# Optimization experiments

Hardware: AMD Instinct MI355X
Metric: run time of the kernel (lower is better)

The kernel has to match this reference:

```python
import jax, jax.numpy as jnp
import numpy as np

N_NODES = 100000
N_EDGES = 1200000
FEAT = 64
AVG_D_LOG = float(np.log(13.0))  # log(avg_degree + 1), avg_degree = 12
EPS_STD = 1e-5   # PNA std epsilon
EPS_BN = 1e-5    # torch BatchNorm1d default eps


def setup_inputs() -> dict:
    key = jax.random.key(0)
    k_h, k_norm, k_src, k_dst = jax.random.split(key, 4)
    h = jax.random.normal(k_h, (N_NODES, FEAT), dtype=jnp.float32)
    norm = jax.random.uniform(k_norm, (N_NODES, 1), dtype=jnp.float32)
    e = jnp.zeros((N_EDGES, 1), dtype=jnp.float32)  # unused by the layer
    src = jax.random.randint(k_src, (N_EDGES,), 0, N_NODES, dtype=jnp.int32)
    dst = jnp.sort(jax.random.randint(k_dst, (N_EDGES,), 0, N_NODES, dtype=jnp.int32))
    bn_weight = jnp.ones((FEAT,), dtype=jnp.float32)
    bn_bias = jnp.zeros((FEAT,), dtype=jnp.float32)
    return {"h": h, "norm": norm, "e": e, "bn_weight": bn_weight,
            "bn_bias": bn_bias, "src": src, "dst": dst}


def reference(h, norm, e, bn_weight, bn_bias, src, dst):
    N, F = h.shape
    hn = h * norm                           # [N, F] pre-scaled node features
    m = hn[src]                             # [E, F] gathered messages (copy_u)

    ones = jnp.ones_like(dst, dtype=hn.dtype)
    deg = jax.ops.segment_sum(ones, dst, num_segments=N, indices_are_sorted=True)  # [N]
    deg_safe = jnp.maximum(deg, 1.0)
    has_nb = (deg > 0)[:, None]             # zero in-degree nodes get zeros (DGL)

    s1 = jax.ops.segment_sum(m, dst, num_segments=N, indices_are_sorted=True)
    s2 = jax.ops.segment_sum(m * m, dst, num_segments=N, indices_are_sorted=True)
    mean = s1 / deg_safe[:, None]
    var = jax.nn.relu(s2 / deg_safe[:, None] - mean * mean)
    std = jnp.sqrt(var + EPS_STD)
    mx = jnp.where(has_nb, jax.ops.segment_max(m, dst, num_segments=N, indices_are_sorted=True), 0.0)
    mn = jnp.where(has_nb, jax.ops.segment_min(m, dst, num_segments=N, indices_are_sorted=True), 0.0)

    agg = jnp.concatenate([mean, mx, mn, std], axis=1)          # [N, 4F]

    logD = jnp.log(deg + 1.0)[:, None]                           # [N, 1]
    amp = agg * (logD / AVG_D_LOG)                               # amplification scaler
    att = agg * (AVG_D_LOG / jnp.where(logD > 0, logD, 1.0))     # attenuation scaler
    scaled = jnp.concatenate([agg, amp, att], axis=1)            # [N, 12F]
    scaled = jnp.where(has_nb, scaled, 0.0)

    out = jnp.concatenate([hn, scaled * norm], axis=1)           # [N, 13F]
    out = out.reshape(N, 13, F).mean(axis=1)                     # [N, F]
    out = jax.nn.relu(out)                                       # activation (dropout p=0)

    # BatchNorm1d, training mode (biased batch variance), affine
    mu = out.mean(axis=0)
    v = out.var(axis=0)
    out = (out - mu) / jnp.sqrt(v + EPS_BN) * bn_weight + bn_bias
    return out
```

## Files before the change

### kernel.cpp

```cpp
#include <hip/hip_runtime.h>
#include <hip/hip_fp16.h>
#include <math.h>
#include <float.h>

#define N_NODES 100000
#define N_EDGES 1200000
#define FEAT 64
#define AVG_D_LOG 2.5649493574615367f
#define EPS_STD 1e-5f
#define EPS_BN 1e-5
#define AGG_BLOCKS 12500
#define HN_BLOCKS 6250
#define RP_BLOCKS 391
#define OLD_RED_BLOCKS 512

#if __has_builtin(__builtin_fmaxf16)
#define H16MAX(a,b) __builtin_fmaxf16((a),(b))
#define H16MIN(a,b) __builtin_fminf16((a),(b))
#else
#define H16MAX(a,b) ((a) > (b) ? (a) : (b))
#define H16MIN(a,b) ((a) < (b) ? (a) : (b))
#endif

__global__ void __launch_bounds__(256) hn_rowptr(
    const float* __restrict__ h, const float* __restrict__ norm,
    const int* __restrict__ dst,
    __half* __restrict__ hn_h, int* __restrict__ rowptr)
{
    const int b = blockIdx.x;
    if (b < HN_BLOCKS) {
        const size_t i4 = ((size_t)b * 256 + threadIdx.x) * 4;
        const int node = (int)(i4 >> 6);
        const float nr = norm[node];
        float4 v = *reinterpret_cast<const float4*>(h + i4);
        __half2 p0 = __floats2half2_rn(v.x * nr, v.y * nr);
        __half2 p1 = __floats2half2_rn(v.z * nr, v.w * nr);
        __half2* o = reinterpret_cast<__half2*>(hn_h + i4);
        o[0] = p0; o[1] = p1;
    } else {
        const int n = (b - HN_BLOCKS) * 256 + threadIdx.x;
        if (n > N_NODES) return;
        int lo = 0, hi = N_EDGES;
        while (lo < hi) {
            int mid = (lo + hi) >> 1;
            if (dst[mid] < n) lo = mid + 1; else hi = mid;
        }
        rowptr[n] = lo;
    }
}

template <bool WRITE_PSTAT>
__global__ void __launch_bounds__(256) pna_agg6(
    const __half* __restrict__ hn, const float* __restrict__ norm,
    const int* __restrict__ src, const int* __restrict__ rowptr,
    float* __restrict__ out, float2* __restrict__ pstat)
{
    const int tid  = threadIdx.x;
    const int wid  = tid >> 6;
    const int lane = tid & 63;
    const int n0   = (blockIdx.x * 4 + wid) * 2;

    const int s0 = __builtin_amdgcn_readfirstlane(rowptr[n0]);
    const int e0 = __builtin_amdgcn_readfirstlane(rowptr[n0 + 1]);
    const int e1 = __builtin_amdgcn_readfirstlane(rowptr[n0 + 2]);
    const int degA = e0 - s0;
    const int degB = e1 - e0;

    const _Float16* __restrict__ hnf = (const _Float16*)hn;
    const float ownA = (float)hnf[(size_t)n0 * FEAT + lane];
    const float ownB = (float)hnf[(size_t)(n0 + 1) * FEAT + lane];

    float s1A = 0.f, s2A = 0.f, s1B = 0.f, s2B = 0.f;
    _Float16 mxA = (_Float16)(-65504.f), mnA = (_Float16)(65504.f);
    _Float16 mxB = (_Float16)(-65504.f), mnB = (_Float16)(65504.f);

#define LOADW(J)  (hnf[(size_t)(J) * FEAT + lane])
#define ACCA(W) do { _Float16 w_ = (W); float f_ = (float)w_;                 \
                     s1A = __builtin_fmaf(f_, 1.0f, s1A);                     \
                     s2A = __builtin_fmaf(f_, f_, s2A);                       \
                     mxA = H16MAX(mxA, w_); mnA = H16MIN(mnA, w_); } while (0)
#define ACCB(W) do { _Float16 w_ = (W); float f_ = (float)w_;                 \
                     s1B = __builtin_fmaf(f_, 1.0f, s1B);                     \
                     s2B = __builtin_fmaf(f_, f_, s2B);                       \
                     mxB = H16MAX(mxB, w_); mnB = H16MIN(mnB, w_); } while (0)

    int ea = s0, eb = e0;
    while (ea + 8 <= e0 && eb + 8 <= e1) {
        const int a0 = src[ea+0], a1 = src[ea+1], a2 = src[ea+2], a3 = src[ea+3];
        const int a4 = src[ea+4], a5 = src[ea+5], a6 = src[ea+6], a7 = src[ea+7];
        const int b0 = src[eb+0], b1 = src[eb+1], b2 = src[eb+2], b3 = src[eb+3];
        const int b4 = src[eb+4], b5 = src[eb+5], b6 = src[eb+6], b7 = src[eb+7];
        _Float16 wa0 = LOADW(a0), wa1 = LOADW(a1), wa2 = LOADW(a2), wa3 = LOADW(a3);
        _Float16 wa4 = LOADW(a4), wa5 = LOADW(a5), wa6 = LOADW(a6), wa7 = LOADW(a7);
        _Float16 wb0 = LOADW(b0), wb1 = LOADW(b1), wb2 = LOADW(b2), wb3 = LOADW(b3);
        _Float16 wb4 = LOADW(b4), wb5 = LOADW(b5), wb6 = LOADW(b6), wb7 = LOADW(b7);
        ACCA(wa0); ACCA(wa1); ACCA(wa2); ACCA(wa3);
        ACCA(wa4); ACCA(wa5); ACCA(wa6); ACCA(wa7);
        ACCB(wb0); ACCB(wb1); ACCB(wb2); ACCB(wb3);
        ACCB(wb4); ACCB(wb5); ACCB(wb6); ACCB(wb7);
        ea += 8; eb += 8;
    }
    while (ea + 4 <= e0 && eb + 4 <= e1) {
        const int a0 = src[ea+0], a1 = src[ea+1], a2 = src[ea+2], a3 = src[ea+3];
        const int b0 = src[eb+0], b1 = src[eb+1], b2 = src[eb+2], b3 = src[eb+3];
        _Float16 wa0 = LOADW(a0), wa1 = LOADW(a1), wa2 = LOADW(a2), wa3 = LOADW(a3);
        _Float16 wb0 = LOADW(b0), wb1 = LOADW(b1), wb2 = LOADW(b2), wb3 = LOADW(b3);
        ACCA(wa0); ACCA(wa1); ACCA(wa2); ACCA(wa3);
        ACCB(wb0); ACCB(wb1); ACCB(wb2); ACCB(wb3);
        ea += 4; eb += 4;
    }
    for (; ea + 4 <= e0; ea += 4) {
        const int a0 = src[ea+0], a1 = src[ea+1], a2 = src[ea+2], a3 = src[ea+3];
        _Float16 w0 = LOADW(a0), w1 = LOADW(a1), w2 = LOADW(a2), w3 = LOADW(a3);
        ACCA(w0); ACCA(w1); ACCA(w2); ACCA(w3);
    }
    for (; ea < e0; ++ea) { _Float16 w = LOADW(src[ea]); ACCA(w); }
    for (; eb + 4 <= e1; eb += 4) {
        const int b0 = src[eb+0], b1 = src[eb+1], b2 = src[eb+2], b3 = src[eb+3];
        _Float16 w0 = LOADW(b0), w1 = LOADW(b1), w2 = LOADW(b2), w3 = LOADW(b3);
        ACCB(w0); ACCB(w1); ACCB(w2); ACCB(w3);
    }
    for (; eb < e1; ++eb) { _Float16 w = LOADW(src[eb]); ACCB(w); }
#undef ACCA
#undef ACCB
#undef LOADW

    float vA, vB;
    {
        float pre;
        if (degA > 0) {
            const float invd = 1.0f / (float)degA;
            const float mean = s1A * invd;
            const float var  = fmaxf(s2A * invd - mean * mean, 0.f);
            const float stdv = sqrtf(var + EPS_STD);
            const float logD = logf((float)degA + 1.0f);
            const float factor = norm[n0] * (1.0f + logD * (1.0f / AVG_D_LOG) + AVG_D_LOG / logD)
                                         * (1.0f / 13.0f);
            pre = ownA * (1.0f / 13.0f) + (mean + (float)mxA + (float)mnA + stdv) * factor;
        } else {
            pre = ownA * (1.0f / 13.0f);
        }
        vA = fmaxf(pre, 0.f);
    }
    {
        float pre;
        if (degB > 0) {
            const float invd = 1.0f / (float)degB;
            const float mean = s1B * invd;
            const float var  = fmaxf(s2B * invd - mean * mean, 0.f);
            const float stdv = sqrtf(var + EPS_STD);
            const float logD = logf((float)degB + 1.0f);
            const float factor = norm[n0 + 1] * (1.0f + logD * (1.0f / AVG_D_LOG) + AVG_D_LOG / logD)
                                             * (1.0f / 13.0f);
            pre = ownB * (1.0f / 13.0f) + (mean + (float)mxB + (float)mnB + stdv) * factor;
        } else {
            pre = ownB * (1.0f / 13.0f);
        }
        vB = fmaxf(pre, 0.f);
    }

    out[(size_t)n0 * FEAT + lane]       = vA;
    out[(size_t)(n0 + 1) * FEAT + lane] = vB;

    if (WRITE_PSTAT) {
        __shared__ float lsS[4][64];
        __shared__ float lsQ[4][64];
        lsS[wid][lane] = vA + vB;
        lsQ[wid][lane] = vA * vA + vB * vB;
        __syncthreads();
        if (tid < 64) {
            float2 p;
            p.x = lsS[0][tid] + lsS[1][tid] + lsS[2][tid] + lsS[3][tid];
            p.y = lsQ[0][tid] + lsQ[1][tid] + lsQ[2][tid] + lsQ[3][tid];
            pstat[(size_t)blockIdx.x * 64 + tid] = p;
        }
    }
}

__global__ void __launch_bounds__(256) bn_stats(
    const float2* __restrict__ pstat,
    const float* __restrict__ w, const float* __restrict__ b,
    float2* __restrict__ ss)
{
    const int f   = (int)blockIdx.x;
    const int tid = threadIdx.x;
    float S = 0.f, Q = 0.f;
    for (int i = tid; i < AGG_BLOCKS; i += 256) {
        float2 p = pstat[(size_t)i * 64 + f];
        S += p.x; Q += p.y;
    }
    __shared__ double rs[256], rq[256];
    rs[tid] = (double)S; rq[tid] = (double)Q;
    __syncthreads();
    for (int s = 128; s > 0; s >>= 1) {
        if (tid < s) { rs[tid] += rs[tid + s]; rq[tid] += rq[tid + s]; }
        __syncthreads();
    }
    if (tid == 0) {
        double mu   = rs[0] / (double)N_NODES;
        double var  = rq[0] / (double)N_NODES - mu * mu;
        double rstd = 1.0 / sqrt(var + EPS_BN);
        float sc = (float)rstd * w[f];
        float2 o; o.x = sc; o.y = b[f] - (float)mu * sc;
        ss[f] = o;
    }
}

__global__ void __launch_bounds__(256) bn_partial(
    const float* __restrict__ out1,
    double* __restrict__ psum, double* __restrict__ psumsq)
{
    const int tid = threadIdx.x;
    const int fb  = tid & 15;
    const int grp = tid >> 4;
    double s0 = 0, s1 = 0, s2 = 0, s3 = 0;
    double q0 = 0, q1 = 0, q2 = 0, q3 = 0;
    for (int n = blockIdx.x * 16 + grp; n < N_NODES; n += OLD_RED_BLOCKS * 16) {
        float4 v = *reinterpret_cast<const float4*>(out1 + (size_t)n * FEAT + fb * 4);
        s0 += (double)v.x; q0 += (double)v.x * (double)v.x;
        s1 += (double)v.y; q1 += (double)v.y * (double)v.y;
        s2 += (double)v.z; q2 += (double)v.z * (double)v.z;
        s3 += (double)v.w; q3 += (double)v.w * (double)v.w;
    }
    __shared__ double ls[256 * 4];
    __shared__ double lq[256 * 4];
    ls[tid * 4 + 0] = s0; ls[tid * 4 + 1] = s1; ls[tid * 4 + 2] = s2; ls[tid * 4 + 3] = s3;
    lq[tid * 4 + 0] = q0; lq[tid * 4 + 1] = q1; lq[tid * 4 + 2] = q2; lq[tid * 4 + 3] = q3;
    __syncthreads();
    if (tid < 64) {
        const int f = tid, fblk = f >> 2, j = f & 3;
        double S = 0, Q = 0;
        for (int g = 0; g < 16; ++g) {
            S += ls[(g * 16 + fblk) * 4 + j];
            Q += lq[(g * 16 + fblk) * 4 + j];
        }
        psum  [blockIdx.x * 64 + f] = S;
        psumsq[blockIdx.x * 64 + f] = Q;
    }
}

__global__ void bn_finalize_old(const double* __restrict__ psum,
                                const double* __restrict__ psumsq,
                                const float* __restrict__ w, const float* __restrict__ b,
                                float2* __restrict__ ss)
{
    int f = threadIdx.x;
    double s = 0.0, s2 = 0.0;
    for (int blk = 0; blk < OLD_RED_BLOCKS; ++blk) {
        s  += psum  [blk * 64 + f];
        s2 += psumsq[blk * 64 + f];
    }
    double mu   = s / (double)N_NODES;
    double var  = s2 / (double)N_NODES - mu * mu;
    double rstd = 1.0 / sqrt(var + EPS_BN);
    float sc = (float)rstd * w[f];
    float2 o; o.x = sc; o.y = b[f] - (float)mu * sc;
    ss[f] = o;
}

__global__ void __launch_bounds__(256) bn_apply2(
    float* __restrict__ out, const float2* __restrict__ ss)
{
    __shared__ float sS[64], sH[64];
    if (threadIdx.x < 64) {
        float2 p = ss[threadIdx.x];
        sS[threadIdx.x] = p.x; sH[threadIdx.x] = p.y;
    }
    __syncthreads();
    const size_t i4 = ((size_t)blockIdx.x * 256 + threadIdx.x) * 4;
    float4 v = *reinterpret_cast<const float4*>(out + i4);
    const int f = (int)(i4 & 63);
    v.x = v.x * sS[f + 0] + sH[f + 0];
    v.y = v.y * sS[f + 1] + sH[f + 1];
    v.z = v.z * sS[f + 2] + sH[f + 2];
    v.w = v.w * sS[f + 3] + sH[f + 3];
    *reinterpret_cast<float4*>(out + i4) = v;
}

extern "C" void kernel_launch(void* const* d_in, const int* in_sizes, int n_in,
                              void* d_out, int out_size, void* d_ws, size_t ws_size,
                              hipStream_t stream) {
    const float* h    = (const float*)d_in[0];
    const float* norm = (const float*)d_in[1];
    const float* bnw  = (const float*)d_in[3];
    const float* bnb  = (const float*)d_in[4];
    const int*   src  = (const int*)d_in[5];
    const int*   dst  = (const int*)d_in[6];
    float* out = (float*)d_out;

    char* ws = (char*)d_ws;
    size_t o = 0;
    __half* hnbuf = (__half*)(ws + o);
    o += (((size_t)N_NODES * FEAT * sizeof(__half)) + 255) & ~(size_t)255;
    int* rowptr = (int*)(ws + o);
    o += (((size_t)(N_NODES + 1) * sizeof(int)) + 255) & ~(size_t)255;
    float2* ss = (float2*)(ws + o); o += 512;
    float2* pstat = (float2*)(ws + o);
    const size_t need_new = o + (size_t)AGG_BLOCKS * 64 * sizeof(float2);
    double* psum   = (double*)(ws + o);
    double* psumsq = (double*)(ws + o + (size_t)OLD_RED_BLOCKS * 64 * sizeof(double));

    hn_rowptr<<<HN_BLOCKS + RP_BLOCKS, 256, 0, stream>>>(h, norm, dst, hnbuf, rowptr);

    if (ws_size >= need_new) {
        pna_agg6<true><<<AGG_BLOCKS, 256, 0, stream>>>(hnbuf, norm, src, rowptr, out, pstat);
        bn_stats<<<64, 256, 0, stream>>>(pstat, bnw, bnb, ss);
    } else {
        pna_agg6<false><<<AGG_BLOCKS, 256, 0, stream>>>(hnbuf, norm, src, rowptr, out, nullptr);
        bn_partial<<<OLD_RED_BLOCKS, 256, 0, stream>>>(out, psum, psumsq);
        bn_finalize_old<<<1, 64, 0, stream>>>(psum, psumsq, bnw, bnb, ss);
    }
    bn_apply2<<<HN_BLOCKS, 256, 0, stream>>>(out, ss);
}
```

Baseline: 88.15 us.

## Build rowptr by edge-boundary scatter and split BN stats into two-stage reduction

Replaces the per-node binary search over dst with a per-edge scan that writes rowptr entries wherever consecutive dst values differ, which removes the log-depth dependent loads. The BN statistics reduction changes from 64 blocks doing strided column reads to 256 blocks reading contiguous rows, followed by a single-block double-precision finalize. This adds one kernel launch, and coalescing improves. The first stage now accumulates in float rather than double, which slightly changes numerics.

New measurement: 84.26 us. -4.4%, faster.

```diff
diff --git a/kernel.cpp b/kernel.cpp
--- a/kernel.cpp
+++ b/kernel.cpp
@@ -11,7 +11,9 @@
 #define EPS_BN 1e-5
 #define AGG_BLOCKS 12500
 #define HN_BLOCKS 6250
-#define RP_BLOCKS 391
+#define SC_BLOCKS 4688
+#define STAT1_BLOCKS 256
+#define ROWS1 49
 #define OLD_RED_BLOCKS 512
 
 #if __has_builtin(__builtin_fmaxf16)
@@ -22,7 +24,7 @@
 #define H16MIN(a,b) ((a) < (b) ? (a) : (b))
 #endif
 
-__global__ void __launch_bounds__(256) hn_rowptr(
+__global__ void __launch_bounds__(256) prep(
     const float* __restrict__ h, const float* __restrict__ norm,
     const int* __restrict__ dst,
     __half* __restrict__ hn_h, int* __restrict__ rowptr)
@@ -38,14 +40,14 @@
         __half2* o = reinterpret_cast<__half2*>(hn_h + i4);
         o[0] = p0; o[1] = p1;
     } else {
-        const int n = (b - HN_BLOCKS) * 256 + threadIdx.x;
-        if (n > N_NODES) return;
-        int lo = 0, hi = N_EDGES;
-        while (lo < hi) {
-            int mid = (lo + hi) >> 1;
-            if (dst[mid] < n) lo = mid + 1; else hi = mid;
-        }
-        rowptr[n] = lo;
+        const int i = (b - HN_BLOCKS) * 256 + threadIdx.x;
+        if (i >= N_EDGES) return;
+        const int d1 = dst[i];
+        const int d0 = (i == 0) ? -1 : dst[i - 1];
+        for (int n = d0 + 1; n <= d1; ++n) rowptr[n] = i;
+        if (i == N_EDGES - 1) {
+            for (int n = d1 + 1; n <= N_NODES; ++n) rowptr[n] = N_EDGES;
+        }
     }
 }
 
@@ -177,32 +179,55 @@
     }
 }
 
-__global__ void __launch_bounds__(256) bn_stats(
-    const float2* __restrict__ pstat,
+__global__ void __launch_bounds__(256) bn_stats1(
+    const float2* __restrict__ pstat, float2* __restrict__ partial)
+{
+    const int tid  = threadIdx.x;
+    const int w    = tid >> 6;
+    const int lane = tid & 63;
+    const int r0 = (int)blockIdx.x * ROWS1;
+    const int r1 = min(r0 + ROWS1, AGG_BLOCKS);
+    float S = 0.f, Q = 0.f;
+    for (int r = r0 + w; r < r1; r += 4) {
+        float2 p = pstat[(size_t)r * 64 + lane];
+        S += p.x; Q += p.y;
+    }
+    __shared__ float sS[4][64], sQ[4][64];
+    sS[w][lane] = S; sQ[w][lane] = Q;
+    __syncthreads();
+    if (tid < 64) {
+        float2 o;
+        o.x = sS[0][tid] + sS[1][tid] + sS[2][tid] + sS[3][tid];
+        o.y = sQ[0][tid] + sQ[1][tid] + sQ[2][tid] + sQ[3][tid];
+        partial[(size_t)blockIdx.x * 64 + tid] = o;
+    }
+}
+
+__global__ void __launch_bounds__(256) bn_stats2(
+    const float2* __restrict__ partial,
     const float* __restrict__ w, const float* __restrict__ b,
     float2* __restrict__ ss)
 {
-    const int f   = (int)blockIdx.x;
     const int tid = threadIdx.x;
-    float S = 0.f, Q = 0.f;
-    for (int i = tid; i < AGG_BLOCKS; i += 256) {
-        float2 p = pstat[(size_t)i * 64 + f];
-        S += p.x; Q += p.y;
-    }
-    __shared__ double rs[256], rq[256];
-    rs[tid] = (double)S; rq[tid] = (double)Q;
+    const int g   = tid >> 6;
+    const int f   = tid & 63;
+    double S = 0.0, Q = 0.0;
+    for (int blk = g; blk < STAT1_BLOCKS; blk += 4) {
+        float2 p = partial[(size_t)blk * 64 + f];
+        S += (double)p.x; Q += (double)p.y;
+    }
+    __shared__ double dS[4][64], dQ[4][64];
+    dS[g][f] = S; dQ[g][f] = Q;
     __syncthreads();
-    for (int s = 128; s > 0; s >>= 1) {
-        if (tid < s) { rs[tid] += rs[tid + s]; rq[tid] += rq[tid + s]; }
-        __syncthreads();
-    }
-    if (tid == 0) {
-        double mu   = rs[0] / (double)N_NODES;
-        double var  = rq[0] / (double)N_NODES - mu * mu;
+    if (tid < 64) {
+        double s = dS[0][tid] + dS[1][tid] + dS[2][tid] + dS[3][tid];
+        double q = dQ[0][tid] + dQ[1][tid] + dQ[2][tid] + dQ[3][tid];
+        double mu   = s / (double)N_NODES;
+        double var  = q / (double)N_NODES - mu * mu;
         double rstd = 1.0 / sqrt(var + EPS_BN);
-        float sc = (float)rstd * w[f];
-        float2 o; o.x = sc; o.y = b[f] - (float)mu * sc;
-        ss[f] = o;
+        float sc = (float)rstd * w[tid];
+        float2 o; o.x = sc; o.y = b[tid] - (float)mu * sc;
+        ss[tid] = o;
     }
 }
 
@@ -295,16 +320,19 @@
     int* rowptr = (int*)(ws + o);
     o += (((size_t)(N_NODES + 1) * sizeof(int)) + 255) & ~(size_t)255;
     float2* ss = (float2*)(ws + o); o += 512;
+    float2* partial = (float2*)(ws + o);
+    o += (size_t)STAT1_BLOCKS * 64 * sizeof(float2);
     float2* pstat = (float2*)(ws + o);
     const size_t need_new = o + (size_t)AGG_BLOCKS * 64 * sizeof(float2);
     double* psum   = (double*)(ws + o);
     double* psumsq = (double*)(ws + o + (size_t)OLD_RED_BLOCKS * 64 * sizeof(double));
 
-    hn_rowptr<<<HN_BLOCKS + RP_BLOCKS, 256, 0, stream>>>(h, norm, dst, hnbuf, rowptr);
+    prep<<<HN_BLOCKS + SC_BLOCKS, 256, 0, stream>>>(h, norm, dst, hnbuf, rowptr);
 
     if (ws_size >= need_new) {
         pna_agg6<true><<<AGG_BLOCKS, 256, 0, stream>>>(hnbuf, norm, src, rowptr, out, pstat);
-        bn_stats<<<64, 256, 0, stream>>>(pstat, bnw, bnb, ss);
+        bn_stats1<<<STAT1_BLOCKS, 256, 0, stream>>>(pstat, partial);
+        bn_stats2<<<1, 256, 0, stream>>>(partial, bnw, bnb, ss);
     } else {
         pna_agg6<false><<<AGG_BLOCKS, 256, 0, stream>>>(hnbuf, norm, src, rowptr, out, nullptr);
         bn_partial<<<OLD_RED_BLOCKS, 256, 0, stream>>>(out, psum, psumsq);
```
